# Kernel tuning notes

Measured on AMD Instinct MI355X. Metric: run time of the kernel, lower is better.

## Reference

```python
import jax, jax.numpy as jnp
from jax import lax
import numpy as np

C_IN, H, W = 9, 11, 11
N_FILT = 64
N_LAYERS = 8
FC_UNITS = 64
LSTM_H = 64
N_ACTIONS = 6
B, T = 32, 128


def setup_inputs() -> dict:
    key = jax.random.key(0)
    ks = jax.random.split(key, 24)
    s = 0.05
    d = {}
    d['x'] = jax.random.normal(ks[0], (B, T, C_IN, H, W), dtype=jnp.float32)
    d['conv0_w'] = jax.random.normal(ks[1], (N_FILT, C_IN, 3, 3), dtype=jnp.float32) * s
    d['conv0_b'] = jnp.zeros((N_FILT,), jnp.float32)
    d['conv_ws'] = jax.random.normal(ks[2], (N_LAYERS - 1, N_FILT, N_FILT, 3, 3), dtype=jnp.float32) * s
    d['conv_bs'] = jnp.zeros((N_LAYERS - 1, N_FILT), jnp.float32)
    d['fc_w'] = jax.random.normal(ks[3], (FC_UNITS, N_FILT * H * W), dtype=jnp.float32) * s
    d['fc_b'] = jnp.zeros((FC_UNITS,), jnp.float32)
    d['w_ih'] = jax.random.normal(ks[4], (4 * LSTM_H, FC_UNITS), dtype=jnp.float32) * s
    d['w_hh'] = jax.random.normal(ks[5], (4 * LSTM_H, LSTM_H), dtype=jnp.float32) * s
    d['b_ih'] = jnp.zeros((4 * LSTM_H,), jnp.float32)
    d['b_hh'] = jnp.zeros((4 * LSTM_H,), jnp.float32)
    d['p1_w'] = jax.random.normal(ks[6], (128, LSTM_H), dtype=jnp.float32) * s
    d['p1_b'] = jnp.zeros((128,), jnp.float32)
    d['p2_w'] = jax.random.normal(ks[7], (N_ACTIONS, 128), dtype=jnp.float32) * s
    d['p2_b'] = jnp.zeros((N_ACTIONS,), jnp.float32)
    d['v1_w'] = jax.random.normal(ks[8], (128, LSTM_H), dtype=jnp.float32) * s
    d['v1_b'] = jnp.zeros((128,), jnp.float32)
    d['v2_w'] = jax.random.normal(ks[9], (1, 128), dtype=jnp.float32) * s
    d['v2_b'] = jnp.zeros((1,), jnp.float32)
    return d


def _conv_relu(h, w, b):
    # h: [N, C, H, W], w: [O, I, 3, 3] -> SAME padding, stride 1
    y = lax.conv_general_dilated(h, w, (1, 1), [(1, 1), (1, 1)],
                                 dimension_numbers=('NCHW', 'OIHW', 'NCHW'))
    return jax.nn.relu(y + b[None, :, None, None])


def _forward(x, conv0_w, conv0_b, conv_ws, conv_bs, fc_w, fc_b,
             w_ih, w_hh, b_ih, b_hh, p1_w, p1_b, p2_w, p2_b, v1_w, v1_b, v2_w, v2_b):
    b, t = x.shape[0], x.shape[1]
    h = x.reshape(b * t, C_IN, H, W)          # batch CNN over all frames at once
    h = _conv_relu(h, conv0_w, conv0_b)
    for i in range(N_LAYERS - 1):             # fixed small layer loop
        h = _conv_relu(h, conv_ws[i], conv_bs[i])
    h = h.reshape(b * t, N_FILT * H * W)
    feats = jax.nn.relu(h @ fc_w.T + fc_b)    # [B*T, FC_UNITS]
    feats = feats.reshape(b, t, FC_UNITS)

    # LSTM (PyTorch gate order i, f, g, o)
    def step(carry, xt):
        hprev, cprev = carry
        g = xt @ w_ih.T + hprev @ w_hh.T + b_ih + b_hh
        i_g, f_g, g_g, o_g = jnp.split(g, 4, axis=-1)
        c = jax.nn.sigmoid(f_g) * cprev + jax.nn.sigmoid(i_g) * jnp.tanh(g_g)
        hn = jax.nn.sigmoid(o_g) * jnp.tanh(c)
        return (hn, c), hn

    h0 = jnp.zeros((b, LSTM_H), feats.dtype)
    c0 = jnp.zeros((b, LSTM_H), feats.dtype)
    _, outs = lax.scan(step, (h0, c0), jnp.swapaxes(feats, 0, 1))  # [T, B, H]
    lstm_out = jnp.swapaxes(outs, 0, 1)       # [B, T, H]

    p = jax.nn.relu(lstm_out @ p1_w.T + p1_b) @ p2_w.T + p2_b  # [B, T, n_actions]
    v = jax.nn.relu(lstm_out @ v1_w.T + v1_b) @ v2_w.T + v2_b  # [B, T, 1]
    return p, v


def reference(x, conv0_w, conv0_b, conv_ws, conv_bs, fc_w, fc_b,
              w_ih, w_hh, b_ih, b_hh, p1_w, p1_b, p2_w, p2_b, v1_w, v1_b, v2_w, v2_b):
    return _forward(x, conv0_w, conv0_b, conv_ws, conv_bs, fc_w, fc_b,
                    w_ih, w_hh, b_ih, b_hh, p1_w, p1_b, p2_w, p2_b,
                    v1_w, v1_b, v2_w, v2_b)
```

## Files before the change

kernel.cpp:

```cpp
#include <hip/hip_runtime.h>
#include <hip/hip_bf16.h>

typedef __attribute__((ext_vector_type(8))) short short8;
typedef __attribute__((ext_vector_type(4))) short short4_t;
typedef __attribute__((ext_vector_type(4))) float floatx4;

#define MFMA_B16(a,b,c) __builtin_amdgcn_mfma_f32_16x16x32_bf16((a),(b),(c),0,0,0)

__device__ __forceinline__ short f2bf(float f) {
    union { __hip_bfloat16 h; short s; } u;
    u.h = __float2bfloat16(f);
    return u.s;
}

union S8U { short4_t h[2]; short8 v; };

#define N_FRAMES 4096
#define C_IN     9
#define POS      121
#define NF       64
#define FC_K     7744
#define ISTR     20
#define FSZ      10816

#define OFF_W0    0
#define OFF_WP    18432
#define OFF_FCP   534528
#define OFF_WIHT  1525760
#define OFF_BSUM  1591296
#define OFF_ACTS  1592320
#define OFF_XG    66079744
#define OFF_HOUT  70274048

__global__ __launch_bounds__(256) void prep_kernel(
    const float* __restrict__ conv0_w, const float* __restrict__ conv_ws,
    const float* __restrict__ w_ih,
    const float* __restrict__ b_ih, const float* __restrict__ b_hh,
    short* __restrict__ w0, short* __restrict__ wpk,
    float* __restrict__ wihT, float* __restrict__ bsum)
{
    int idx = blockIdx.x*256 + threadIdx.x;
    if (idx < 9216) {
        int o9 = idx >> 10; int r = idx & 1023; int o = r >> 4; int ci = r & 15;
        float v = (ci < 9) ? conv0_w[(o*9 + ci)*9 + o9] : 0.f;
        w0[idx] = f2bf(v);
        return;
    }
    idx -= 9216;
    if (idx < 258048) {
        int l = idx / 36864; int r = idx % 36864; int o9 = r >> 12; int rr = r & 4095;
        int o = rr >> 6; int ci = rr & 63;
        wpk[idx] = f2bf(conv_ws[((l*64 + o)*64 + ci)*9 + o9]);
        return;
    }
    idx -= 258048;
    if (idx < 16384) {
        int k = idx >> 8; int g = idx & 255;
        wihT[idx] = w_ih[g*64 + k];
        return;
    }
    idx -= 16384;
    if (idx < 256) bsum[idx] = b_ih[idx] + b_hh[idx];
}

__global__ __launch_bounds__(256) void fc_transpose(
    const float* __restrict__ fc_w, short* __restrict__ fcp)
{
    __shared__ float row[FC_K];
    const int u = blockIdx.x;
    const int tid = threadIdx.x;
    const float* src = fc_w + (size_t)u*FC_K;
    for (int i = tid; i < FC_K; i += 256) row[i] = src[i];
    __syncthreads();
    short* dst = fcp + (size_t)u*FC_K;
    for (int k2 = tid; k2 < FC_K; k2 += 256) {
        int p = k2 >> 6, c = k2 & 63;
        dst[k2] = f2bf(row[c*121 + p]);
    }
}

__global__ __launch_bounds__(256) void conv_stack(
    const float* __restrict__ x,
    const float* __restrict__ conv0_b,
    const float* __restrict__ conv_bs,
    const short* __restrict__ w0,
    const short* __restrict__ wpk,
    short* __restrict__ acts_out)
{
    __shared__ alignas(16) short act[2*FSZ];
    const int tid  = threadIdx.x;
    const int lane = tid & 63;
    const int w    = tid >> 6;
    const int fr   = w >> 1;
    const int mh   = w & 1;
    const int m    = lane & 15;
    const int kg   = lane >> 4;
    const int ht   = tid & 127;
    const int hf   = tid >> 7;

    short* actf = act + fr*FSZ;
    char*  actb = (char*)actf;

    const short8 zero8 = {0,0,0,0,0,0,0,0};
    const floatx4 fzero = {0.f,0.f,0.f,0.f};

    {
        short* ab = act + hf*FSZ;
        for (int i = ht*8; i < 3392; i += 1024) *(short8*)(&ab[i]) = zero8;
    }
    __syncthreads();

    {
        short* ab = act + hf*FSZ;
        const float* xf = x + (size_t)(blockIdx.x*2 + hf)*(C_IN*POS);
        for (int i = ht; i < C_IN*POS; i += 128) {
            int ci = i / POS;
            int p  = i - ci*POS;
            int yy = p / 11;
            int xx = p - yy*11;
            ab[((yy+1)*13 + (xx+1))*ISTR + ci] = f2bf(xf[i]);
        }
    }
    __syncthreads();

    floatx4 acc[2][8];
    #pragma unroll
    for (int mt=0;mt<2;mt++)
        #pragma unroll
        for (int j=0;j<8;j++) acc[mt][j] = fzero;

    int cellA[8], vbase[8];
    #pragma unroll
    for (int j = 0; j < 8; ++j) {
        int p = j*16 + m;
        int pc = (p <= 120) ? p : 120;
        int yy = pc / 11, xx = pc - yy*11;
        cellA[j] = yy*13 + xx;
        vbase[j] = cellA[j]*128;
    }

    {
        const bool kz  = (kg >= 2);
        const int  kgl = (kg & 1)*8;
        const short* w0w = w0 + (mh*32 + m)*16 + kgl;
        #pragma unroll 1
        for (int dy = 0; dy < 3; ++dy) {
            #pragma unroll 1
            for (int dx = 0; dx < 3; ++dx) {
                const short* w9 = w0w + (dy*3+dx)*1024;
                const int so = (dy*13+dx)*ISTR + kgl;
                short8 a[2];
                #pragma unroll
                for (int mt=0;mt<2;mt++) {
                    short8 t = *(const short8*)(w9 + mt*256);
                    a[mt] = kz ? zero8 : t;
                }
                #pragma unroll
                for (int j=0;j<8;j++) {
                    const short* bp = actf + cellA[j]*ISTR + so;
                    S8U t;
                    t.h[0] = *(const short4_t*)(bp);
                    t.h[1] = *(const short4_t*)(bp + 4);
                    short8 b = t.v;
                    #pragma unroll
                    for (int mt=0;mt<2;mt++)
                        acc[mt][j] = MFMA_B16(a[mt], b, acc[mt][j]);
                }
            }
        }
    }

    __syncthreads();
    {
        short* ab = act + hf*FSZ;
        for (int i = ht*8; i < FSZ; i += 1024) *(short8*)(&ab[i]) = zero8;
    }
    __syncthreads();

    auto epilogue = [&](const float* bias) {
        __syncthreads();
        #pragma unroll
        for (int mt=0;mt<2;mt++) {
            const int ch0 = mh*32 + mt*16 + kg*4;
            const int gw  = ch0 >> 3;
            const int off = 1792 + (((gw + m) & 7)<<4) + (kg&1)*8;
            floatx4 bb = *(const floatx4*)(bias + ch0);
            #pragma unroll
            for (int j=0;j<8;j++) {
                floatx4 v = acc[mt][j];
                acc[mt][j] = fzero;
                int p = j*16 + m;
                if (p > 120) continue;
                short4_t sv;
                sv.x = f2bf(fmaxf(v.x + bb.x, 0.f));
                sv.y = f2bf(fmaxf(v.y + bb.y, 0.f));
                sv.z = f2bf(fmaxf(v.z + bb.z, 0.f));
                sv.w = f2bf(fmaxf(v.w + bb.w, 0.f));
                *(short4_t*)(actb + vbase[j] + off) = sv;
            }
        }
        __syncthreads();
    };

    epilogue(conv0_b);

    for (int l = 1; l < 8; ++l) {
        const short* wl = wpk + (l-1)*36864 + (mh*32 + m)*64 + kg*8;
        #pragma unroll 1
        for (int dy = 0; dy < 3; ++dy) {
            #pragma unroll 1
            for (int dx = 0; dx < 3; ++dx) {
                const short* wo = wl + (dy*3+dx)*4096;
                const int sb = (dy*13+dx)*128;
                const int cu = dy*11 + dx + 4 + kg + m;
                #pragma unroll 1
                for (int kc = 0; kc < 2; ++kc) {
                    short8 a[2];
                    #pragma unroll
                    for (int mt=0;mt<2;mt++)
                        a[mt] = *(const short8*)(wo + mt*1024 + kc*32);
                    const int soff = sb + (((cu + kc*4) & 7)<<4);
                    #pragma unroll
                    for (int j=0;j<8;j++) {
                        short8 b = *(const short8*)(actb + vbase[j] + soff);
                        #pragma unroll
                        for (int mt=0;mt<2;mt++)
                            acc[mt][j] = MFMA_B16(a[mt], b, acc[mt][j]);
                    }
                }
            }
        }
        epilogue(conv_bs + (l-1)*NF);
    }

    {
        const char* ab = (const char*)(act + hf*FSZ);
        short* dst = acts_out + (size_t)(blockIdx.x*2 + hf)*FC_K;
        for (int it = 0; it < 8; ++it) {
            int q = ht + it*128;
            if (q < 968) {
                int p = q >> 3, G = q & 7;
                int yy = p / 11, xx = p - yy*11;
                int cell = (yy+1)*13 + (xx+1);
                int slot = (G + p) & 7;
                short8 v = *(const short8*)(ab + cell*128 + slot*16);
                *(short8*)(dst + q*8) = v;
            }
        }
    }
}

__global__ __launch_bounds__(256) void fc_xg_kernel(
    const short* __restrict__ acts, const short* __restrict__ fcp,
    const float* __restrict__ fc_b, const float* __restrict__ wihT,
    const float* __restrict__ bsum, float* __restrict__ xg)
{
    __shared__ alignas(16) float red[3*64*16];
    __shared__ alignas(16) float fbuf[16*64];
    const int tid  = threadIdx.x;
    const int lane = tid & 63;
    const int w    = tid >> 6;
    const int m    = lane & 15;
    const int kg   = lane >> 4;
    const int bm   = blockIdx.x;

    const floatx4 fzero = {0.f,0.f,0.f,0.f};
    floatx4 acc[4];
    #pragma unroll
    for (int nt=0;nt<4;nt++) acc[nt] = fzero;

    const short* arow = acts + (size_t)(bm*16 + m)*FC_K + kg*8;
    const short* brow = fcp + (size_t)m*FC_K + kg*8;

    for (int kc = w; kc < 242; kc += 4) {
        short8 a = *(const short8*)(arow + kc*32);
        #pragma unroll
        for (int nt=0;nt<4;nt++) {
            short8 b = *(const short8*)(brow + (size_t)nt*16*FC_K + kc*32);
            acc[nt] = MFMA_B16(a, b, acc[nt]);
        }
    }

    if (w > 0) {
        #pragma unroll
        for (int nt=0;nt<4;nt++)
            *(floatx4*)(&red[((w-1)*64 + lane)*16 + nt*4]) = acc[nt];
    }
    __syncthreads();
    if (w == 0) {
        #pragma unroll
        for (int nt=0;nt<4;nt++)
            for (int j=0;j<3;j++)
                acc[nt] += *(const floatx4*)(&red[(j*64 + lane)*16 + nt*4]);
        #pragma unroll
        for (int nt=0;nt<4;nt++) {
            int unit = nt*16 + m;
            float bias = fc_b[unit];
            int fr = kg*4;
            fbuf[(fr+0)*NF + unit] = fmaxf(acc[nt].x + bias, 0.f);
            fbuf[(fr+1)*NF + unit] = fmaxf(acc[nt].y + bias, 0.f);
            fbuf[(fr+2)*NF + unit] = fmaxf(acc[nt].z + bias, 0.f);
            fbuf[(fr+3)*NF + unit] = fmaxf(acc[nt].w + bias, 0.f);
        }
    }
    __syncthreads();

    {
        const int g = tid;
        float a[16];
        float bs = bsum[g];
        #pragma unroll
        for (int i=0;i<16;i++) a[i] = bs;
        for (int k=0;k<64;k++) {
            float wk = wihT[k*256 + g];
            #pragma unroll
            for (int i=0;i<16;i++) a[i] += fbuf[i*64 + k] * wk;
        }
        float* xo = xg + (size_t)(bm*16)*256 + g;
        #pragma unroll
        for (int i=0;i<16;i++) xo[i*256] = a[i];
    }
}

__device__ __forceinline__ float sigmf_(float v){ return 1.f/(1.f + __expf(-v)); }

__global__ __launch_bounds__(128) void lstm_kernel(
    const float* __restrict__ xg, const float* __restrict__ whh,
    float* __restrict__ hout)
{
    __shared__ alignas(16) float hbuf[64];
    __shared__ alignas(16) float gbuf[256];
    const int t = threadIdx.x;
    const int b = blockIdx.x;

    float4 w0v[16], w1v[16];
    #pragma unroll
    for (int k=0;k<16;k++) w0v[k] = *(const float4*)(whh + t*64 + k*4);
    #pragma unroll
    for (int k=0;k<16;k++) w1v[k] = *(const float4*)(whh + (t+128)*64 + k*4);

    float c = 0.f;
    if (t < 64) hbuf[t] = 0.f;
    __syncthreads();

    const float* xr = xg + (size_t)(b*128)*256;
    float nA = xr[t];
    float nB = xr[t+128];

    for (int ts=0; ts<128; ++ts) {
        float aA = nA, aB = nB;
        if (ts + 1 < 128) {
            const float* xn = xr + (ts+1)*256;
            nA = xn[t];
            nB = xn[t+128];
        }
        #pragma unroll
        for (int k=0;k<16;k++) {
            float4 hv = *(const float4*)(&hbuf[k*4]);
            aA += hv.x*w0v[k].x + hv.y*w0v[k].y + hv.z*w0v[k].z + hv.w*w0v[k].w;
            aB += hv.x*w1v[k].x + hv.y*w1v[k].y + hv.z*w1v[k].z + hv.w*w1v[k].w;
        }
        gbuf[t] = aA;
        gbuf[t+128] = aB;
        __syncthreads();
        if (t < 64) {
            float ig = sigmf_(gbuf[t]);
            float fg = sigmf_(gbuf[64+t]);
            float gg = tanhf(gbuf[128+t]);
            float og = sigmf_(gbuf[192+t]);
            c = fg*c + ig*gg;
            float h = og*tanhf(c);
            hbuf[t] = h;
            hout[(b*128+ts)*64 + t] = h;
        }
        __syncthreads();
    }
}

__global__ __launch_bounds__(64) void heads_kernel(
    const float* __restrict__ hout,
    const float* __restrict__ p1w, const float* __restrict__ p1b,
    const float* __restrict__ p2w, const float* __restrict__ p2b,
    const float* __restrict__ v1w, const float* __restrict__ v1b,
    const float* __restrict__ v2w, const float* __restrict__ v2b,
    float* __restrict__ out)
{
    __shared__ alignas(16) float hbuf[64];
    __shared__ alignas(16) float a1[128];
    __shared__ alignas(16) float a2[128];
    const int lane = threadIdx.x;
    for (int fi=0; fi<4; ++fi) {
        const int f = blockIdx.x*4 + fi;
        hbuf[lane] = hout[f*64 + lane];
        __syncthreads();
        #pragma unroll
        for (int uu=0; uu<2; ++uu) {
            const int u = lane + uu*64;
            float s1 = p1b[u], s2 = v1b[u];
            const float4* wp1 = (const float4*)(p1w + u*64);
            const float4* wv1 = (const float4*)(v1w + u*64);
            #pragma unroll
            for (int k=0;k<16;k++) {
                float4 h4 = *(const float4*)(&hbuf[k*4]);
                float4 w4 = wp1[k];
                s1 += h4.x*w4.x + h4.y*w4.y + h4.z*w4.z + h4.w*w4.w;
                float4 q4 = wv1[k];
                s2 += h4.x*q4.x + h4.y*q4.y + h4.z*q4.z + h4.w*q4.w;
            }
            a1[u] = fmaxf(s1, 0.f);
            a2[u] = fmaxf(s2, 0.f);
        }
        __syncthreads();
        if (lane < 6) {
            float s = p2b[lane];
            const float* wr = p2w + lane*128;
            #pragma unroll
            for (int j=0;j<128;j++) s += a1[j]*wr[j];
            out[f*6 + lane] = s;
        }
        if (lane == 6) {
            float s = v2b[0];
            #pragma unroll
            for (int j=0;j<128;j++) s += a2[j]*v2w[j];
            out[24576 + f] = s;
        }
        __syncthreads();
    }
}

extern "C" void kernel_launch(void* const* d_in, const int* in_sizes, int n_in,
                              void* d_out, int out_size, void* d_ws, size_t ws_size,
                              hipStream_t stream) {
    const float* x       = (const float*)d_in[0];
    const float* conv0_w = (const float*)d_in[1];
    const float* conv0_b = (const float*)d_in[2];
    const float* conv_ws = (const float*)d_in[3];
    const float* conv_bs = (const float*)d_in[4];
    const float* fc_w    = (const float*)d_in[5];
    const float* fc_b    = (const float*)d_in[6];
    const float* w_ih    = (const float*)d_in[7];
    const float* w_hh    = (const float*)d_in[8];
    const float* b_ih    = (const float*)d_in[9];
    const float* b_hh    = (const float*)d_in[10];
    const float* p1_w    = (const float*)d_in[11];
    const float* p1_b    = (const float*)d_in[12];
    const float* p2_w    = (const float*)d_in[13];
    const float* p2_b    = (const float*)d_in[14];
    const float* v1_w    = (const float*)d_in[15];
    const float* v1_b    = (const float*)d_in[16];
    const float* v2_w    = (const float*)d_in[17];
    const float* v2_b    = (const float*)d_in[18];
    float* out = (float*)d_out;

    char* ws = (char*)d_ws;
    short* w0    = (short*)(ws + OFF_W0);
    short* wpk   = (short*)(ws + OFF_WP);
    short* fcp   = (short*)(ws + OFF_FCP);
    float* wihT  = (float*)(ws + OFF_WIHT);
    float* bsum  = (float*)(ws + OFF_BSUM);
    short* acts  = (short*)(ws + OFF_ACTS);
    float* xgb   = (float*)(ws + OFF_XG);
    float* hout  = (float*)(ws + OFF_HOUT);

    prep_kernel<<<1109, 256, 0, stream>>>(conv0_w, conv_ws, w_ih, b_ih, b_hh,
                                          w0, wpk, wihT, bsum);
    fc_transpose<<<64, 256, 0, stream>>>(fc_w, fcp);
    conv_stack<<<N_FRAMES/2, 256, 0, stream>>>(x, conv0_b, conv_bs, w0, wpk, acts);
    fc_xg_kernel<<<256, 256, 0, stream>>>(acts, fcp, fc_b, wihT, bsum, xgb);
    lstm_kernel<<<32, 128, 0, stream>>>(xgb, w_hh, hout);
    heads_kernel<<<1024, 64, 0, stream>>>(hout, p1_w, p1_b, p2_w, p2_b,
                                          v1_w, v1_b, v2_w, v2_b, out);
}
```

Measured before the change: 573.8 us.

## Split conv work by spatial tiles per wave and use fast LSTM activations

Each wave in the conv stack now computes all 64 output channels for half of the spatial tiles, instead of half the channels for all tiles. Each activation fragment loaded from LDS is then reused across four weight tiles, which halves activation LDS reads, but each wave now loads twice as many weight fragments from global memory. Separately, the LSTM gate nonlinearities switch to hardware reciprocal and an exp-based tanh, shortening the serial recurrence at a small accuracy cost.

```diff
diff --git a/kernel.cpp b/kernel.cpp
--- a/kernel.cpp
+++ b/kernel.cpp
@@ -92,7 +92,7 @@
     const int lane = tid & 63;
     const int w    = tid >> 6;
     const int fr   = w >> 1;
-    const int mh   = w & 1;
+    const int nh   = w & 1;
     const int m    = lane & 15;
     const int kg   = lane >> 4;
     const int ht   = tid & 127;
@@ -123,48 +123,48 @@
     }
     __syncthreads();
 
-    floatx4 acc[2][8];
+    floatx4 acc[4][4];
     #pragma unroll
-    for (int mt=0;mt<2;mt++)
-        #pragma unroll
-        for (int j=0;j<8;j++) acc[mt][j] = fzero;
-
-    int cellA[8], vbase[8];
+    for (int mt=0;mt<4;mt++)
+        #pragma unroll
+        for (int jj=0;jj<4;jj++) acc[mt][jj] = fzero;
+
+    int cellA[4], vbase[4];
     #pragma unroll
-    for (int j = 0; j < 8; ++j) {
-        int p = j*16 + m;
+    for (int jj = 0; jj < 4; ++jj) {
+        int p = (nh*4 + jj)*16 + m;
         int pc = (p <= 120) ? p : 120;
         int yy = pc / 11, xx = pc - yy*11;
-        cellA[j] = yy*13 + xx;
-        vbase[j] = cellA[j]*128;
+        cellA[jj] = yy*13 + xx;
+        vbase[jj] = cellA[jj]*128;
     }
 
     {
         const bool kz  = (kg >= 2);
         const int  kgl = (kg & 1)*8;
-        const short* w0w = w0 + (mh*32 + m)*16 + kgl;
+        const short* w0w = w0 + m*16 + kgl;
         #pragma unroll 1
         for (int dy = 0; dy < 3; ++dy) {
             #pragma unroll 1
             for (int dx = 0; dx < 3; ++dx) {
                 const short* w9 = w0w + (dy*3+dx)*1024;
                 const int so = (dy*13+dx)*ISTR + kgl;
-                short8 a[2];
+                short8 a[4];
                 #pragma unroll
-                for (int mt=0;mt<2;mt++) {
+                for (int mt=0;mt<4;mt++) {
                     short8 t = *(const short8*)(w9 + mt*256);
                     a[mt] = kz ? zero8 : t;
                 }
                 #pragma unroll
-                for (int j=0;j<8;j++) {
-                    const short* bp = actf + cellA[j]*ISTR + so;
+                for (int jj=0;jj<4;jj++) {
+                    const short* bp = actf + cellA[jj]*ISTR + so;
                     S8U t;
                     t.h[0] = *(const short4_t*)(bp);
                     t.h[1] = *(const short4_t*)(bp + 4);
                     short8 b = t.v;
                     #pragma unroll
-                    for (int mt=0;mt<2;mt++)
-                        acc[mt][j] = MFMA_B16(a[mt], b, acc[mt][j]);
+                    for (int mt=0;mt<4;mt++)
+                        acc[mt][jj] = MFMA_B16(a[mt], b, acc[mt][jj]);
                 }
             }
         }
@@ -180,23 +180,23 @@
     auto epilogue = [&](const float* bias) {
         __syncthreads();
         #pragma unroll
-        for (int mt=0;mt<2;mt++) {
-            const int ch0 = mh*32 + mt*16 + kg*4;
+        for (int mt=0;mt<4;mt++) {
+            const int ch0 = mt*16 + kg*4;
             const int gw  = ch0 >> 3;
             const int off = 1792 + (((gw + m) & 7)<<4) + (kg&1)*8;
             floatx4 bb = *(const floatx4*)(bias + ch0);
             #pragma unroll
-            for (int j=0;j<8;j++) {
-                floatx4 v = acc[mt][j];
-                acc[mt][j] = fzero;
-                int p = j*16 + m;
+            for (int jj=0;jj<4;jj++) {
+                floatx4 v = acc[mt][jj];
+                acc[mt][jj] = fzero;
+                int p = (nh*4 + jj)*16 + m;
                 if (p > 120) continue;
                 short4_t sv;
                 sv.x = f2bf(fmaxf(v.x + bb.x, 0.f));
                 sv.y = f2bf(fmaxf(v.y + bb.y, 0.f));
                 sv.z = f2bf(fmaxf(v.z + bb.z, 0.f));
                 sv.w = f2bf(fmaxf(v.w + bb.w, 0.f));
-                *(short4_t*)(actb + vbase[j] + off) = sv;
+                *(short4_t*)(actb + vbase[jj] + off) = sv;
             }
         }
         __syncthreads();
@@ -205,7 +205,7 @@
     epilogue(conv0_b);
 
     for (int l = 1; l < 8; ++l) {
-        const short* wl = wpk + (l-1)*36864 + (mh*32 + m)*64 + kg*8;
+        const short* wl = wpk + (l-1)*36864 + m*64 + kg*8;
         #pragma unroll 1
         for (int dy = 0; dy < 3; ++dy) {
             #pragma unroll 1
@@ -215,17 +215,17 @@
                 const int cu = dy*11 + dx + 4 + kg + m;
                 #pragma unroll 1
                 for (int kc = 0; kc < 2; ++kc) {
-                    short8 a[2];
+                    short8 a[4];
                     #pragma unroll
-                    for (int mt=0;mt<2;mt++)
+                    for (int mt=0;mt<4;mt++)
                         a[mt] = *(const short8*)(wo + mt*1024 + kc*32);
                     const int soff = sb + (((cu + kc*4) & 7)<<4);
                     #pragma unroll
-                    for (int j=0;j<8;j++) {
-                        short8 b = *(const short8*)(actb + vbase[j] + soff);
+                    for (int jj=0;jj<4;jj++) {
+                        short8 b = *(const short8*)(actb + vbase[jj] + soff);
                         #pragma unroll
-                        for (int mt=0;mt<2;mt++)
-                            acc[mt][j] = MFMA_B16(a[mt], b, acc[mt][j]);
+                        for (int mt=0;mt<4;mt++)
+                            acc[mt][jj] = MFMA_B16(a[mt], b, acc[mt][jj]);
                     }
                 }
             }
@@ -322,7 +322,12 @@
     }
 }
 
-__device__ __forceinline__ float sigmf_(float v){ return 1.f/(1.f + __expf(-v)); }
+__device__ __forceinline__ float sigmf_(float v){
+    return __builtin_amdgcn_rcpf(1.f + __expf(-v));
+}
+__device__ __forceinline__ float tanhf_(float v){
+    return 1.f - 2.f*__builtin_amdgcn_rcpf(__expf(2.f*v) + 1.f);
+}
 
 __global__ __launch_bounds__(128) void lstm_kernel(
     const float* __restrict__ xg, const float* __restrict__ whh,
@@ -366,10 +371,10 @@
         if (t < 64) {
             float ig = sigmf_(gbuf[t]);
             float fg = sigmf_(gbuf[64+t]);
-            float gg = tanhf(gbuf[128+t]);
+            float gg = tanhf_(gbuf[128+t]);
             float og = sigmf_(gbuf[192+t]);
             c = fg*c + ig*gg;
-            float h = og*tanhf(c);
+            float h = og*tanhf_(c);
             hbuf[t] = h;
             hout[(b*128+ts)*64 + t] = h;
         }
```

Result: slower. 757.8 us (+32.1%).
